# Performance work log

Hardware: AMD Instinct MI355X
Metric: run time of the kernel (lower is better)

## Reference

```python
import jax, jax.numpy as jnp
import numpy as np

B, S, D, F, E, K = 4, 2048, 1024, 4096, 8, 1


def setup_inputs() -> dict:
    key = jax.random.key(0)
    ks = jax.random.split(key, 4)
    sc = lambda n: 1.0 / np.sqrt(n)
    return {
        "hidden_states": jax.random.normal(ks[0], (B, S, D), jnp.float32),
        "gate_w": jax.random.normal(ks[1], (E, D), jnp.float32) * sc(D),
        "w1": jax.random.normal(ks[2], (E, F, D), jnp.float32) * sc(D),
        "b1": jnp.zeros((E, F), jnp.float32),
        "w2": jax.random.normal(ks[3], (E, D, F), jnp.float32) * sc(F),
        "b2": jnp.zeros((E, D), jnp.float32),
    }


def moe_forward(hidden_states, gate_w, w1, b1, w2, b2, k=K):
    b, s, d = hidden_states.shape
    e = gate_w.shape[0]
    x = hidden_states.reshape(-1, d)  # [T, D]
    router_logits = x @ gate_w.T  # [T, E]
    router_probs = jax.nn.softmax(router_logits.astype(jnp.float32), axis=-1)
    topw, sel = jax.lax.top_k(router_probs, k)  # [T, k]
    topw = topw / topw.sum(axis=-1, keepdims=True)
    topw = topw.astype(x.dtype)

    # router z-loss: sum(logsumexp(logits)^2) / T
    log_z = jax.scipy.special.logsumexp(router_logits.astype(jnp.float32), axis=-1)
    z_loss = jnp.sum(log_z ** 2) / x.shape[0]

    # load balancing loss (torch code: one_hot(sel).max(-2) -> [T,E])
    router_prob_per_expert = jnp.mean(topw.astype(jnp.float32), axis=-2)  # [k]
    expert_mask = jax.nn.one_hot(sel, e, dtype=jnp.int32).max(axis=-2)  # [T, E]
    tokens_per_expert = jnp.mean(expert_mask.astype(jnp.float32), axis=-2)  # [E]
    aux_loss = jnp.mean(tokens_per_expert * router_prob_per_expert) * (e ** 2)

    # combine weights [T, E]: routing weight where expert selected, else 0
    combine = (jax.nn.one_hot(sel, e, dtype=x.dtype) * topw[..., None]).sum(axis=1)

    out = jnp.zeros_like(x)
    for ei in range(e):  # fixed small expert loop (structurally distinct params)
        h = jax.nn.gelu(x @ w1[ei].T + b1[ei])  # [T, F]
        y = h @ w2[ei].T + b2[ei]  # [T, D]
        out = out + combine[:, ei:ei + 1] * y
    return out.reshape(b, s, d), aux_loss, z_loss


def reference(hidden_states, gate_w, w1, b1, w2, b2):
    return moe_forward(hidden_states, gate_w, w1, b1, w2, b2)
```

## Files before the change

kernel.cpp:

```cpp
#include <hip/hip_runtime.h>
#include <hip/hip_bf16.h>
#include <stdint.h>

#define TOK 8192
#define DD 1024
#define FF 4096
#define EE 8
#define BM 128
#define BN 128
#define BK 64
#define MT_MAX 72

typedef __attribute__((ext_vector_type(8))) short bf16x8;
typedef __attribute__((ext_vector_type(4))) float f32x4;

#define WS_SEL    0u
#define WS_CNT    32768u
#define WS_CUR    (32768u + 64u)
#define WS_TSTART (32768u + 128u)
#define WS_ZSUM   (32768u + 192u)
#define WS_PERM   33024u
#define WS_XB     131072u
#define WS_H      (131072u + 16777216u)

__device__ __forceinline__ unsigned short f2bf(float f) {
  unsigned int u = __builtin_bit_cast(unsigned int, f);
  u = (u + 0x7FFFu + ((u >> 16) & 1u)) >> 16;
  return (unsigned short)u;
}

__device__ __forceinline__ void async_copy16(const void* g, void* l) {
  __builtin_amdgcn_global_load_lds(
      (const __attribute__((address_space(1))) unsigned int*)g,
      (__attribute__((address_space(3))) unsigned int*)l, 16, 0, 0);
}

__global__ __launch_bounds__(256) void k_router(const float* __restrict__ x,
                                                const float* __restrict__ gw,
                                                uint8_t* __restrict__ ws) {
  const int wv = threadIdx.x >> 6, l = threadIdx.x & 63;
  const int t = (int)blockIdx.x * 4 + wv;
  int* sel = (int*)(ws + WS_SEL);
  int* cnt = (int*)(ws + WS_CNT);
  float* zsum = (float*)(ws + WS_ZSUM);
  unsigned short* xb = (unsigned short*)(ws + WS_XB);
  const float4* xr = (const float4*)(x + (size_t)t * DD);
  double acc[EE];
#pragma unroll
  for (int e = 0; e < EE; ++e) acc[e] = 0.0;
#pragma unroll
  for (int i = 0; i < 4; ++i) {
    const int idx = l + i * 64;
    const float4 v = xr[idx];
    ushort4 b;
    b.x = f2bf(v.x); b.y = f2bf(v.y); b.z = f2bf(v.z); b.w = f2bf(v.w);
    *(ushort4*)(xb + (size_t)t * DD + (size_t)idx * 4) = b;
#pragma unroll
    for (int e = 0; e < EE; ++e) {
      const float4 g = ((const float4*)(gw + (size_t)e * DD))[idx];
      acc[e] += (double)v.x * g.x + (double)v.y * g.y +
                (double)v.z * g.z + (double)v.w * g.w;
    }
  }
#pragma unroll
  for (int e = 0; e < EE; ++e) {
#pragma unroll
    for (int s = 32; s > 0; s >>= 1) acc[e] += __shfl_xor(acc[e], s, 64);
  }
  if (l == 0) {
    double m = acc[0]; int am = 0;
#pragma unroll
    for (int e = 1; e < EE; ++e) if (acc[e] > m) { m = acc[e]; am = e; }
    float se = 0.f;
#pragma unroll
    for (int e = 0; e < EE; ++e) se += __expf((float)(acc[e] - m));
    const float lse = (float)m + __logf(se);
    sel[t] = am;
    atomicAdd(cnt + am, 1);
    atomicAdd(zsum, lse * lse);
  }
}

__global__ void k_finalize(uint8_t* __restrict__ ws, float* __restrict__ out) {
  if (threadIdx.x != 0 || blockIdx.x != 0) return;
  int* cnt = (int*)(ws + WS_CNT);
  int* cur = (int*)(ws + WS_CUR);
  int* ts = (int*)(ws + WS_TSTART);
  int tiles = 0, s = 0;
  for (int e = 0; e < EE; ++e) {
    ts[e] = tiles;
    cur[e] = tiles * BM;
    tiles += (cnt[e] + BM - 1) / BM;
    s += cnt[e];
  }
  ts[EE] = tiles;
  const float zs = *(float*)(ws + WS_ZSUM);
  out[(size_t)TOK * DD] = (float)EE * ((float)s / (float)TOK);
  out[(size_t)TOK * DD + 1] = zs / (float)TOK;
}

__global__ __launch_bounds__(256) void k_scatter(uint8_t* __restrict__ ws) {
  const int t = (int)blockIdx.x * 256 + threadIdx.x;
  if (t >= TOK) return;
  const int e = ((const int*)(ws + WS_SEL))[t];
  const int pos = atomicAdd((int*)(ws + WS_CUR) + e, 1);
  ((int*)(ws + WS_PERM))[pos] = t;
}

template <int K, int NTOT, bool DOGELU, bool INDIRECT>
__global__ __launch_bounds__(256) void k_gemm(const unsigned short* __restrict__ A,
                                              const float* __restrict__ W,
                                              const float* __restrict__ bias,
                                              uint8_t* __restrict__ ws,
                                              float* __restrict__ out) {
  const int* ts = (const int*)(ws + WS_TSTART);
  const int* perm = (const int*)(ws + WS_PERM);
  unsigned short* H = (unsigned short*)(ws + WS_H);

  const int MT = (int)gridDim.x;
  const int nblk = MT * (int)gridDim.y;
  const int orig = (int)blockIdx.y * MT + (int)blockIdx.x;
  const int q = nblk >> 3, r = nblk & 7;
  const int xcd = orig & 7, b8 = orig >> 3;
  const int wg = (xcd < r ? xcd * (q + 1) : r * (q + 1) + (xcd - r) * q) + b8;
  const int mt = wg % MT, nt = wg / MT;

  const int total = ts[EE];
  if (mt >= total) return;
  int e = 0;
#pragma unroll
  for (int i = 1; i < EE; ++i) if (mt >= ts[i]) e = i;

  const int m0 = mt * BM, n0 = nt * BN;
  const float* Wb = W + (size_t)e * NTOT * K;
  const float* bs = bias + (size_t)e * NTOT;

  __shared__ __align__(16) unsigned short As[BM * BK];
  __shared__ __align__(16) unsigned short Bs[BN * BK];

  const int tid = threadIdx.x, wv = tid >> 6, l = tid & 63;
  const int wr = wv >> 1, wc = wv & 1;

  f32x4 acc[4][4];
#pragma unroll
  for (int m = 0; m < 4; ++m)
#pragma unroll
    for (int n = 0; n < 4; ++n) acc[m][n] = f32x4{0.f, 0.f, 0.f, 0.f};

  int arow[4];
#pragma unroll
  for (int j = 0; j < 4; ++j) {
    const int row = (tid + j * 256) >> 3;
    if (INDIRECT) {
      const int tk = perm[m0 + row];
      arow[j] = tk < 0 ? 0 : tk;
    } else {
      arow[j] = m0 + row;
    }
  }

  for (int k0 = 0; k0 < K; k0 += BK) {
#pragma unroll
    for (int j = 0; j < 4; ++j) {
      const int p = tid + j * 256;
      const int row = p >> 3, pc = p & 7;
      const int lc = pc ^ (row & 7);
      const unsigned short* src = A + (size_t)arow[j] * K + k0 + lc * 8;
      async_copy16(src, (char*)As + (size_t)(j * 256 + wv * 64) * 16);
    }
#pragma unroll
    for (int i = 0; i < 8; ++i) {
      const int c = tid + i * 256;
      const int row = c >> 4, cc = c & 15;
      const float4 v = *(const float4*)(Wb + (size_t)(n0 + row) * K + k0 + cc * 4);
      uint2 u;
      u.x = (unsigned)f2bf(v.x) | ((unsigned)f2bf(v.y) << 16);
      u.y = (unsigned)f2bf(v.z) | ((unsigned)f2bf(v.w) << 16);
      const int phys = row * 128 + (((cc >> 1) ^ (row & 7)) << 4) + ((cc & 1) << 3);
      *(uint2*)((char*)Bs + phys) = u;
    }
    __syncthreads();
#pragma unroll
    for (int kk = 0; kk < 2; ++kk) {
      const int ch = kk * 4 + (l >> 4);
      bf16x8 af[4], bfr[4];
#pragma unroll
      for (int m = 0; m < 4; ++m) {
        const int row = wr * 64 + m * 16 + (l & 15);
        af[m] = *(const bf16x8*)((const char*)As + row * 128 + ((ch ^ (row & 7)) << 4));
      }
#pragma unroll
      for (int n = 0; n < 4; ++n) {
        const int row = wc * 64 + n * 16 + (l & 15);
        bfr[n] = *(const bf16x8*)((const char*)Bs + row * 128 + ((ch ^ (row & 7)) << 4));
      }
#pragma unroll
      for (int m = 0; m < 4; ++m)
#pragma unroll
        for (int n = 0; n < 4; ++n)
          acc[m][n] = __builtin_amdgcn_mfma_f32_16x16x32_bf16(af[m], bfr[n], acc[m][n], 0, 0, 0);
    }
    __syncthreads();
  }

  const int cl = l & 15, rg = l >> 4;
#pragma unroll
  for (int n = 0; n < 4; ++n) {
    const int col = n0 + wc * 64 + n * 16 + cl;
    const float bv = bs[col];
#pragma unroll
    for (int m = 0; m < 4; ++m) {
      const int rbase = m0 + wr * 64 + m * 16 + rg * 4;
#pragma unroll
      for (int qq = 0; qq < 4; ++qq) {
        const int rr = rbase + qq;
        float v = acc[m][n][qq] + bv;
        if (DOGELU) {
          const float u0 = 0.7978845608028654f * (v + 0.044715f * v * v * v);
          const float th = 1.f - 2.f / (__expf(2.f * u0) + 1.f);
          v = 0.5f * v * (1.f + th);
          H[(size_t)rr * FF + col] = f2bf(v);
        } else {
          const int tk = perm[rr];
          if (tk >= 0) out[(size_t)tk * DD + col] = v;
        }
      }
    }
  }
}

extern "C" void kernel_launch(void* const* d_in, const int* in_sizes, int n_in,
                              void* d_out, int out_size, void* d_ws, size_t ws_size,
                              hipStream_t stream) {
  const float* x = (const float*)d_in[0];
  const float* gw = (const float*)d_in[1];
  const float* w1 = (const float*)d_in[2];
  const float* b1 = (const float*)d_in[3];
  const float* w2 = (const float*)d_in[4];
  const float* b2 = (const float*)d_in[5];
  float* out = (float*)d_out;
  uint8_t* ws = (uint8_t*)d_ws;

  hipMemsetAsync(ws + WS_CNT, 0, 256, stream);
  hipMemsetAsync(ws + WS_PERM, 0xFF, MT_MAX * BM * 4, stream);

  k_router<<<TOK / 4, 256, 0, stream>>>(x, gw, ws);
  k_finalize<<<1, 64, 0, stream>>>(ws, out);
  k_scatter<<<TOK / 256, 256, 0, stream>>>(ws);

  const unsigned short* Xb = (const unsigned short*)(ws + WS_XB);
  const unsigned short* Hb = (const unsigned short*)(ws + WS_H);
  k_gemm<DD, FF, true, true><<<dim3(MT_MAX, FF / BN), 256, 0, stream>>>(Xb, w1, b1, ws, out);
  k_gemm<FF, DD, false, false><<<dim3(MT_MAX, DD / BN), 256, 0, stream>>>(Hb, w2, b2, ws, out);
}
```

Baseline: 821.3 us.

## Pre-convert expert weights to bf16 and split-K the second GEMM

Adds a conversion kernel that turns w1 and w2 into bf16 copies in the workspace on every call. The GEMMs can then stage weight tiles with async global-to-LDS copies instead of per-tile fp32 loads and in-register conversion, which also halves the bytes of repeated weight reads. The second GEMM is split along K into two halves whose results are combined with atomicAdd into an output zeroed beforehand, to put more blocks on the GPU. The cost is an extra pass over all weights, roughly 200MB of extra workspace (with a fallback to the old fp32 path when the workspace is too small), and float atomics that make the output summation order nondeterministic.

```diff
diff --git a/kernel.cpp b/kernel.cpp
--- a/kernel.cpp
+++ b/kernel.cpp
@@ -21,7 +21,10 @@
 #define WS_ZSUM   (32768u + 192u)
 #define WS_PERM   33024u
 #define WS_XB     131072u
-#define WS_H      (131072u + 16777216u)
+#define WS_H      (WS_XB + 16777216u)
+#define WS_W1B    (WS_H + 75497472u)
+#define WS_W2B    (WS_W1B + 67108864u)
+#define WS_NEED   ((size_t)WS_W2B + 67108864u)
 
 __device__ __forceinline__ unsigned short f2bf(float f) {
   unsigned int u = __builtin_bit_cast(unsigned int, f);
@@ -33,6 +36,17 @@
   __builtin_amdgcn_global_load_lds(
       (const __attribute__((address_space(1))) unsigned int*)g,
       (__attribute__((address_space(3))) unsigned int*)l, 16, 0, 0);
+}
+
+__global__ __launch_bounds__(256) void k_convert(const float* __restrict__ src,
+                                                 unsigned short* __restrict__ dst,
+                                                 int n4) {
+  for (int i = (int)blockIdx.x * 256 + threadIdx.x; i < n4; i += (int)gridDim.x * 256) {
+    const float4 v = ((const float4*)src)[i];
+    ushort4 b;
+    b.x = f2bf(v.x); b.y = f2bf(v.y); b.z = f2bf(v.z); b.w = f2bf(v.w);
+    ((ushort4*)dst)[i] = b;
+  }
 }
 
 __global__ __launch_bounds__(256) void k_router(const float* __restrict__ x,
@@ -107,9 +121,10 @@
   ((int*)(ws + WS_PERM))[pos] = t;
 }
 
-template <int K, int NTOT, bool DOGELU, bool INDIRECT>
+template <int K, int NTOT, int KSPLIT, bool DOGELU, bool INDIRECT, bool BF16B>
 __global__ __launch_bounds__(256) void k_gemm(const unsigned short* __restrict__ A,
-                                              const float* __restrict__ W,
+                                              const float* __restrict__ Wf,
+                                              const unsigned short* __restrict__ Wb,
                                               const float* __restrict__ bias,
                                               uint8_t* __restrict__ ws,
                                               float* __restrict__ out) {
@@ -118,21 +133,23 @@
   unsigned short* H = (unsigned short*)(ws + WS_H);
 
   const int MT = (int)gridDim.x;
+  const int NT = NTOT / BN;
   const int nblk = MT * (int)gridDim.y;
   const int orig = (int)blockIdx.y * MT + (int)blockIdx.x;
   const int q = nblk >> 3, r = nblk & 7;
   const int xcd = orig & 7, b8 = orig >> 3;
   const int wg = (xcd < r ? xcd * (q + 1) : r * (q + 1) + (xcd - r) * q) + b8;
-  const int mt = wg % MT, nt = wg / MT;
-
-  const int total = ts[EE];
-  if (mt >= total) return;
+  const int mt = wg % MT;
+  const int rest = wg / MT;
+  const int nt = rest % NT;
+  const int kh = rest / NT;
+
+  if (mt >= ts[EE]) return;
   int e = 0;
 #pragma unroll
   for (int i = 1; i < EE; ++i) if (mt >= ts[i]) e = i;
 
   const int m0 = mt * BM, n0 = nt * BN;
-  const float* Wb = W + (size_t)e * NTOT * K;
   const float* bs = bias + (size_t)e * NTOT;
 
   __shared__ __align__(16) unsigned short As[BM * BK];
@@ -159,25 +176,38 @@
     }
   }
 
-  for (int k0 = 0; k0 < K; k0 += BK) {
+  const int kbeg = kh * (K / KSPLIT), kend = kbeg + K / KSPLIT;
+  for (int k0 = kbeg; k0 < kend; k0 += BK) {
 #pragma unroll
     for (int j = 0; j < 4; ++j) {
       const int p = tid + j * 256;
       const int row = p >> 3, pc = p & 7;
       const int lc = pc ^ (row & 7);
-      const unsigned short* src = A + (size_t)arow[j] * K + k0 + lc * 8;
-      async_copy16(src, (char*)As + (size_t)(j * 256 + wv * 64) * 16);
-    }
-#pragma unroll
-    for (int i = 0; i < 8; ++i) {
-      const int c = tid + i * 256;
-      const int row = c >> 4, cc = c & 15;
-      const float4 v = *(const float4*)(Wb + (size_t)(n0 + row) * K + k0 + cc * 4);
-      uint2 u;
-      u.x = (unsigned)f2bf(v.x) | ((unsigned)f2bf(v.y) << 16);
-      u.y = (unsigned)f2bf(v.z) | ((unsigned)f2bf(v.w) << 16);
-      const int phys = row * 128 + (((cc >> 1) ^ (row & 7)) << 4) + ((cc & 1) << 3);
-      *(uint2*)((char*)Bs + phys) = u;
+      async_copy16(A + (size_t)arow[j] * K + k0 + lc * 8,
+                   (char*)As + (size_t)(j * 256 + wv * 64) * 16);
+    }
+    if (BF16B) {
+#pragma unroll
+      for (int j = 0; j < 4; ++j) {
+        const int p = tid + j * 256;
+        const int row = p >> 3, pc = p & 7;
+        const int lc = pc ^ (row & 7);
+        async_copy16(Wb + (size_t)e * NTOT * K + (size_t)(n0 + row) * K + k0 + lc * 8,
+                     (char*)Bs + (size_t)(j * 256 + wv * 64) * 16);
+      }
+    } else {
+#pragma unroll
+      for (int i = 0; i < 8; ++i) {
+        const int c = tid + i * 256;
+        const int row = c >> 4, cc = c & 15;
+        const float4 v = *(const float4*)(Wf + (size_t)e * NTOT * K +
+                                          (size_t)(n0 + row) * K + k0 + cc * 4);
+        uint2 u;
+        u.x = (unsigned)f2bf(v.x) | ((unsigned)f2bf(v.y) << 16);
+        u.y = (unsigned)f2bf(v.z) | ((unsigned)f2bf(v.w) << 16);
+        const int phys = row * 128 + (((cc >> 1) ^ (row & 7)) << 4) + ((cc & 1) << 3);
+        *(uint2*)((char*)Bs + phys) = u;
+      }
     }
     __syncthreads();
 #pragma unroll
@@ -207,7 +237,7 @@
 #pragma unroll
   for (int n = 0; n < 4; ++n) {
     const int col = n0 + wc * 64 + n * 16 + cl;
-    const float bv = bs[col];
+    const float bv = (KSPLIT == 1 || kh == 0) ? bs[col] : 0.f;
 #pragma unroll
     for (int m = 0; m < 4; ++m) {
       const int rbase = m0 + wr * 64 + m * 16 + rg * 4;
@@ -222,7 +252,10 @@
           H[(size_t)rr * FF + col] = f2bf(v);
         } else {
           const int tk = perm[rr];
-          if (tk >= 0) out[(size_t)tk * DD + col] = v;
+          if (tk >= 0) {
+            if (KSPLIT == 1) out[(size_t)tk * DD + col] = v;
+            else atomicAdd(out + (size_t)tk * DD + col, v);
+          }
         }
       }
     }
@@ -240,9 +273,18 @@
   const float* b2 = (const float*)d_in[5];
   float* out = (float*)d_out;
   uint8_t* ws = (uint8_t*)d_ws;
+  const bool full = ws_size >= WS_NEED;
 
   hipMemsetAsync(ws + WS_CNT, 0, 256, stream);
   hipMemsetAsync(ws + WS_PERM, 0xFF, MT_MAX * BM * 4, stream);
+  hipMemsetAsync(out, 0, (size_t)TOK * DD * 4, stream);
+
+  unsigned short* w1b = (unsigned short*)(ws + WS_W1B);
+  unsigned short* w2b = (unsigned short*)(ws + WS_W2B);
+  if (full) {
+    k_convert<<<2048, 256, 0, stream>>>(w1, w1b, EE * FF * DD / 4);
+    k_convert<<<2048, 256, 0, stream>>>(w2, w2b, EE * DD * FF / 4);
+  }
 
   k_router<<<TOK / 4, 256, 0, stream>>>(x, gw, ws);
   k_finalize<<<1, 64, 0, stream>>>(ws, out);
@@ -250,6 +292,15 @@
 
   const unsigned short* Xb = (const unsigned short*)(ws + WS_XB);
   const unsigned short* Hb = (const unsigned short*)(ws + WS_H);
-  k_gemm<DD, FF, true, true><<<dim3(MT_MAX, FF / BN), 256, 0, stream>>>(Xb, w1, b1, ws, out);
-  k_gemm<FF, DD, false, false><<<dim3(MT_MAX, DD / BN), 256, 0, stream>>>(Hb, w2, b2, ws, out);
-}
+  if (full) {
+    k_gemm<DD, FF, 1, true, true, true>
+        <<<dim3(MT_MAX, FF / BN), 256, 0, stream>>>(Xb, w1, w1b, b1, ws, out);
+    k_gemm<FF, DD, 2, false, false, true>
+        <<<dim3(MT_MAX, (DD / BN) * 2), 256, 0, stream>>>(Hb, w2, w2b, b2, ws, out);
+  } else {
+    k_gemm<DD, FF, 1, true, true, false>
+        <<<dim3(MT_MAX, FF / BN), 256, 0, stream>>>(Xb, w1, w1b, b1, ws, out);
+    k_gemm<FF, DD, 2, false, false, false>
+        <<<dim3(MT_MAX, (DD / BN) * 2), 256, 0, stream>>>(Hb, w2, w2b, b2, ws, out);
+  }
+}
```

Result: slower. 863.2 us (+5.1%).

## Pre-convert weights to bf16, use double-buffered 256x256 tiles, split-K second GEMM

Applied to the files above, without the earlier changes.

Adds a conversion kernel that turns each expert weight tensor into bf16 in workspace once per call. Before this, every GEMM block converted fp32 weights on the fly, repeating the work for every token tile. The GEMM now uses 256x256 tiles with 512 threads and a double-buffered LDS pipeline, loading both operands through async global-to-LDS copies. The second GEMM splits K four ways and combines partial results with atomic adds into an output that is zeroed first. The cost is extra weight conversion traffic, roughly 128KB of LDS per block which limits occupancy, and atomic contention on the output.

```diff
diff --git a/kernel.cpp b/kernel.cpp
--- a/kernel.cpp
+++ b/kernel.cpp
@@ -6,22 +6,24 @@
 #define DD 1024
 #define FF 4096
 #define EE 8
-#define BM 128
-#define BN 128
+#define BM 256
+#define BN 256
 #define BK 64
-#define MT_MAX 72
+#define NW 512
+#define MT_MAX 40
 
 typedef __attribute__((ext_vector_type(8))) short bf16x8;
 typedef __attribute__((ext_vector_type(4))) float f32x4;
 
 #define WS_SEL    0u
 #define WS_CNT    32768u
-#define WS_CUR    (32768u + 64u)
-#define WS_TSTART (32768u + 128u)
-#define WS_ZSUM   (32768u + 192u)
+#define WS_CUR    32832u
+#define WS_TSTART 32896u
+#define WS_ZSUM   32960u
 #define WS_PERM   33024u
 #define WS_XB     131072u
-#define WS_H      (131072u + 16777216u)
+#define WS_H      (WS_XB + 16777216u)
+#define WS_WB     (WS_H + 83886080u)
 
 __device__ __forceinline__ unsigned short f2bf(float f) {
   unsigned int u = __builtin_bit_cast(unsigned int, f);
@@ -33,6 +35,17 @@
   __builtin_amdgcn_global_load_lds(
       (const __attribute__((address_space(1))) unsigned int*)g,
       (__attribute__((address_space(3))) unsigned int*)l, 16, 0, 0);
+}
+
+__global__ __launch_bounds__(256) void k_convert(const float* __restrict__ src,
+                                                 unsigned short* __restrict__ dst,
+                                                 int n4) {
+  for (int i = (int)blockIdx.x * 256 + threadIdx.x; i < n4; i += (int)gridDim.x * 256) {
+    const float4 v = ((const float4*)src)[i];
+    ushort4 b;
+    b.x = f2bf(v.x); b.y = f2bf(v.y); b.z = f2bf(v.z); b.w = f2bf(v.w);
+    ((ushort4*)dst)[i] = b;
+  }
 }
 
 __global__ __launch_bounds__(256) void k_router(const float* __restrict__ x,
@@ -107,110 +120,119 @@
   ((int*)(ws + WS_PERM))[pos] = t;
 }
 
-template <int K, int NTOT, bool DOGELU, bool INDIRECT>
-__global__ __launch_bounds__(256) void k_gemm(const unsigned short* __restrict__ A,
-                                              const float* __restrict__ W,
-                                              const float* __restrict__ bias,
-                                              uint8_t* __restrict__ ws,
-                                              float* __restrict__ out) {
+template <int K, int NTOT, int KSPLIT, bool DOGELU, bool INDIRECT>
+__global__ __launch_bounds__(NW, 2) void k_gemm256(const unsigned short* __restrict__ A,
+                                                   const unsigned short* __restrict__ W,
+                                                   const float* __restrict__ bias,
+                                                   uint8_t* __restrict__ ws,
+                                                   float* __restrict__ out) {
   const int* ts = (const int*)(ws + WS_TSTART);
   const int* perm = (const int*)(ws + WS_PERM);
   unsigned short* H = (unsigned short*)(ws + WS_H);
 
   const int MT = (int)gridDim.x;
+  const int NT = NTOT / BN;
   const int nblk = MT * (int)gridDim.y;
   const int orig = (int)blockIdx.y * MT + (int)blockIdx.x;
   const int q = nblk >> 3, r = nblk & 7;
   const int xcd = orig & 7, b8 = orig >> 3;
   const int wg = (xcd < r ? xcd * (q + 1) : r * (q + 1) + (xcd - r) * q) + b8;
-  const int mt = wg % MT, nt = wg / MT;
-
-  const int total = ts[EE];
-  if (mt >= total) return;
+  const int mt = wg % MT;
+  const int rest = wg / MT;
+  const int nt = rest % NT;
+  const int kh = rest / NT;
+
+  if (mt >= ts[EE]) return;
   int e = 0;
 #pragma unroll
   for (int i = 1; i < EE; ++i) if (mt >= ts[i]) e = i;
 
   const int m0 = mt * BM, n0 = nt * BN;
-  const float* Wb = W + (size_t)e * NTOT * K;
+  const unsigned short* We = W + (size_t)e * NTOT * K;
   const float* bs = bias + (size_t)e * NTOT;
 
-  __shared__ __align__(16) unsigned short As[BM * BK];
-  __shared__ __align__(16) unsigned short Bs[BN * BK];
-
-  const int tid = threadIdx.x, wv = tid >> 6, l = tid & 63;
-  const int wr = wv >> 1, wc = wv & 1;
-
-  f32x4 acc[4][4];
-#pragma unroll
-  for (int m = 0; m < 4; ++m)
+  __shared__ __align__(16) unsigned short sm[2][2][BM * BK];
+
+  const int tid = threadIdx.x, wid = tid >> 6, l = tid & 63;
+  const int wr = wid >> 2, wc = wid & 3;
+
+  f32x4 acc[8][4];
+#pragma unroll
+  for (int m = 0; m < 8; ++m)
 #pragma unroll
     for (int n = 0; n < 4; ++n) acc[m][n] = f32x4{0.f, 0.f, 0.f, 0.f};
 
-  int arow[4];
+  int arow[4], brow[4];
 #pragma unroll
   for (int j = 0; j < 4; ++j) {
-    const int row = (tid + j * 256) >> 3;
+    const int row = (tid + j * NW) >> 3;
     if (INDIRECT) {
       const int tk = perm[m0 + row];
       arow[j] = tk < 0 ? 0 : tk;
     } else {
       arow[j] = m0 + row;
     }
-  }
-
-  for (int k0 = 0; k0 < K; k0 += BK) {
+    brow[j] = n0 + row;
+  }
+
+  const int kbeg = kh * (K / KSPLIT);
+  const int NS = (K / KSPLIT) / BK;
+
+  auto stage = [&](int buf, int k0) {
 #pragma unroll
     for (int j = 0; j < 4; ++j) {
-      const int p = tid + j * 256;
+      const int p = tid + j * NW;
       const int row = p >> 3, pc = p & 7;
       const int lc = pc ^ (row & 7);
-      const unsigned short* src = A + (size_t)arow[j] * K + k0 + lc * 8;
-      async_copy16(src, (char*)As + (size_t)(j * 256 + wv * 64) * 16);
-    }
-#pragma unroll
-    for (int i = 0; i < 8; ++i) {
-      const int c = tid + i * 256;
-      const int row = c >> 4, cc = c & 15;
-      const float4 v = *(const float4*)(Wb + (size_t)(n0 + row) * K + k0 + cc * 4);
-      uint2 u;
-      u.x = (unsigned)f2bf(v.x) | ((unsigned)f2bf(v.y) << 16);
-      u.y = (unsigned)f2bf(v.z) | ((unsigned)f2bf(v.w) << 16);
-      const int phys = row * 128 + (((cc >> 1) ^ (row & 7)) << 4) + ((cc & 1) << 3);
-      *(uint2*)((char*)Bs + phys) = u;
-    }
-    __syncthreads();
+      async_copy16(A + (size_t)arow[j] * K + k0 + lc * 8,
+                   (char*)&sm[buf][0][0] + (size_t)p * 16);
+      async_copy16(We + (size_t)brow[j] * K + k0 + lc * 8,
+                   (char*)&sm[buf][1][0] + (size_t)p * 16);
+    }
+  };
+
+  stage(0, kbeg);
+  asm volatile("s_waitcnt vmcnt(0)" ::: "memory");
+  __syncthreads();
+
+  int cur = 0;
+  for (int t = 0; t < NS; ++t) {
+    if (t + 1 < NS) stage(cur ^ 1, kbeg + (t + 1) * BK);
+    const char* Ab = (const char*)&sm[cur][0][0];
+    const char* Bb = (const char*)&sm[cur][1][0];
 #pragma unroll
     for (int kk = 0; kk < 2; ++kk) {
       const int ch = kk * 4 + (l >> 4);
-      bf16x8 af[4], bfr[4];
-#pragma unroll
-      for (int m = 0; m < 4; ++m) {
-        const int row = wr * 64 + m * 16 + (l & 15);
-        af[m] = *(const bf16x8*)((const char*)As + row * 128 + ((ch ^ (row & 7)) << 4));
+      bf16x8 af[8], bf_[4];
+#pragma unroll
+      for (int m = 0; m < 8; ++m) {
+        const int row = wr * 128 + m * 16 + (l & 15);
+        af[m] = *(const bf16x8*)(Ab + row * 128 + ((ch ^ (row & 7)) << 4));
       }
 #pragma unroll
       for (int n = 0; n < 4; ++n) {
         const int row = wc * 64 + n * 16 + (l & 15);
-        bfr[n] = *(const bf16x8*)((const char*)Bs + row * 128 + ((ch ^ (row & 7)) << 4));
+        bf_[n] = *(const bf16x8*)(Bb + row * 128 + ((ch ^ (row & 7)) << 4));
       }
 #pragma unroll
-      for (int m = 0; m < 4; ++m)
+      for (int m = 0; m < 8; ++m)
 #pragma unroll
         for (int n = 0; n < 4; ++n)
-          acc[m][n] = __builtin_amdgcn_mfma_f32_16x16x32_bf16(af[m], bfr[n], acc[m][n], 0, 0, 0);
-    }
+          acc[m][n] = __builtin_amdgcn_mfma_f32_16x16x32_bf16(af[m], bf_[n], acc[m][n], 0, 0, 0);
+    }
+    asm volatile("s_waitcnt vmcnt(0)" ::: "memory");
     __syncthreads();
+    cur ^= 1;
   }
 
   const int cl = l & 15, rg = l >> 4;
 #pragma unroll
   for (int n = 0; n < 4; ++n) {
     const int col = n0 + wc * 64 + n * 16 + cl;
-    const float bv = bs[col];
-#pragma unroll
-    for (int m = 0; m < 4; ++m) {
-      const int rbase = m0 + wr * 64 + m * 16 + rg * 4;
+    const float bv = (KSPLIT == 1 || kh == 0) ? bs[col] : 0.f;
+#pragma unroll
+    for (int m = 0; m < 8; ++m) {
+      const int rbase = m0 + wr * 128 + m * 16 + rg * 4;
 #pragma unroll
       for (int qq = 0; qq < 4; ++qq) {
         const int rr = rbase + qq;
@@ -222,7 +244,10 @@
           H[(size_t)rr * FF + col] = f2bf(v);
         } else {
           const int tk = perm[rr];
-          if (tk >= 0) out[(size_t)tk * DD + col] = v;
+          if (tk >= 0) {
+            if (KSPLIT == 1) out[(size_t)tk * DD + col] = v;
+            else atomicAdd(out + (size_t)tk * DD + col, v);
+          }
         }
       }
     }
@@ -243,13 +268,22 @@
 
   hipMemsetAsync(ws + WS_CNT, 0, 256, stream);
   hipMemsetAsync(ws + WS_PERM, 0xFF, MT_MAX * BM * 4, stream);
-
+  hipMemsetAsync(out, 0, (size_t)TOK * DD * 4, stream);
+
+  unsigned short* wb = (unsigned short*)(ws + WS_WB);
+  const unsigned short* Xb = (const unsigned short*)(ws + WS_XB);
+  const unsigned short* Hb = (const unsigned short*)(ws + WS_H);
+
+  k_convert<<<2048, 256, 0, stream>>>(w1, wb, EE * FF * DD / 4);
   k_router<<<TOK / 4, 256, 0, stream>>>(x, gw, ws);
   k_finalize<<<1, 64, 0, stream>>>(ws, out);
   k_scatter<<<TOK / 256, 256, 0, stream>>>(ws);
 
-  const unsigned short* Xb = (const unsigned short*)(ws + WS_XB);
-  const unsigned short* Hb = (const unsigned short*)(ws + WS_H);
-  k_gemm<DD, FF, true, true><<<dim3(MT_MAX, FF / BN), 256, 0, stream>>>(Xb, w1, b1, ws, out);
-  k_gemm<FF, DD, false, false><<<dim3(MT_MAX, DD / BN), 256, 0, stream>>>(Hb, w2, b2, ws, out);
-}
+  k_gemm256<DD, FF, 1, true, true>
+      <<<dim3(MT_MAX, FF / BN), NW, 0, stream>>>(Xb, wb, b1, ws, out);
+
+  k_convert<<<2048, 256, 0, stream>>>(w2, wb, EE * DD * FF / 4);
+
+  k_gemm256<FF, DD, 4, false, false>
+      <<<dim3(MT_MAX, (DD / BN) * 4), NW, 0, stream>>>(Hb, wb, b2, ws, out);
+}
```

After: 824.5 us. About the same (+0.4%).
